# Kernel optimization log

Measured on AMD Instinct MI355X. Metric: run time of the kernel, lower is better.

The kernel has to match this reference:

```python
import jax, jax.numpy as jnp
import numpy as np

B, LX, LM, D = 4, 512, 512, 256

def setup_inputs() -> dict:
    key = jax.random.key(0)
    ks = jax.random.split(key, 7)
    s = 1.0 / np.sqrt(D)
    return {
        "x": jax.random.normal(ks[0], (B, LX, D), jnp.float32),
        "memory": jax.random.normal(ks[1], (B, LM, D), jnp.float32),
        "memory_mask": jax.random.randint(ks[2], (B, LM), 0, 2, jnp.int32),
        "W1": jax.random.normal(ks[3], (D, D), jnp.float32) * s,
        "b1": jax.random.normal(ks[4], (D,), jnp.float32) * s,
        "W2": jax.random.normal(ks[5], (D, D), jnp.float32) * s,
        "Wt": jax.random.normal(ks[6], (D,), jnp.float32) * s,
    }

def reference(x, memory, memory_mask, W1, b1, W2, Wt):
    # item1: (B, Lx, D); item2: (B, Lm, D)
    item1 = jnp.einsum("bxd,ed->bxe", x, W1) + b1
    item2 = jnp.einsum("bmd,ed->bme", memory, W2)
    # additive attention: tanh of broadcast sum, then reduce D to scalar logit
    item = item1[:, :, None, :] + item2[:, None, :, :]  # (B, Lx, Lm, D)
    S_logit = jnp.einsum("bxmd,d->bxm", jnp.tanh(item), Wt)
    S_logit = jnp.where(memory_mask[:, None, :] == 0, jnp.float32(-10000.0), S_logit)
    return S_logit
```

## Files before the change

kernel.cpp:

```cpp
#include <hip/hip_runtime.h>

namespace {

constexpr int B = 4, LX = 512, LM = 512, D = 256;
constexpr float KSCALE = 2.8853900817779268f;
constexpr float CLAMP = 15.0f;

typedef __attribute__((ext_vector_type(8))) short short8;
typedef __attribute__((ext_vector_type(4))) float f32x4;

__device__ __forceinline__ short f2bf_rne(float f) {
    unsigned u = __float_as_uint(f);
    u += 0x7FFFu + ((u >> 16) & 1u);
    return (short)(u >> 16);
}

__global__ __launch_bounds__(256) void proj_mfma(
    const float* __restrict__ x, const float* __restrict__ mem,
    const float* __restrict__ W1, const float* __restrict__ b1,
    const float* __restrict__ W2, float* __restrict__ E1, float* __restrict__ E2)
{
    const int tid  = threadIdx.x;
    const int wv   = tid >> 6;
    const int lane = tid & 63;
    const int tile = blockIdx.x * 4 + wv;
    const int z    = tile >> 11;
    const int t    = tile & 2047;
    const int r0   = (t >> 4) << 4;
    const int e0   = (t & 15) << 4;
    const int lr   = lane & 15;
    const int quad = lane >> 4;

    const float* __restrict__ A = (z ? mem : x) + (size_t)(r0 + lr) * D + quad * 8;
    const float* __restrict__ W = (z ? W2 : W1) + (size_t)(e0 + lr) * D + quad * 8;

    f32x4 acc = {0.f, 0.f, 0.f, 0.f};
#pragma unroll
    for (int kc = 0; kc < D; kc += 32) {
        float4 a0 = *(const float4*)(A + kc);
        float4 a1 = *(const float4*)(A + kc + 4);
        float4 w0 = *(const float4*)(W + kc);
        float4 w1 = *(const float4*)(W + kc + 4);
        short8 af, bf;
        af[0] = f2bf_rne(a0.x); af[1] = f2bf_rne(a0.y);
        af[2] = f2bf_rne(a0.z); af[3] = f2bf_rne(a0.w);
        af[4] = f2bf_rne(a1.x); af[5] = f2bf_rne(a1.y);
        af[6] = f2bf_rne(a1.z); af[7] = f2bf_rne(a1.w);
        bf[0] = f2bf_rne(w0.x); bf[1] = f2bf_rne(w0.y);
        bf[2] = f2bf_rne(w0.z); bf[3] = f2bf_rne(w0.w);
        bf[4] = f2bf_rne(w1.x); bf[5] = f2bf_rne(w1.y);
        bf[6] = f2bf_rne(w1.z); bf[7] = f2bf_rne(w1.w);
        acc = __builtin_amdgcn_mfma_f32_16x16x32_bf16(af, bf, acc, 0, 0, 0);
    }

    float* __restrict__ E = z ? E2 : E1;
    const float bias = z ? 0.f : b1[e0 + lr];
#pragma unroll
    for (int reg = 0; reg < 4; ++reg) {
        const int row = quad * 4 + reg;
        float arg = KSCALE * (acc[reg] + bias);
        arg = fminf(fmaxf(arg, -CLAMP), CLAMP);
        E[(size_t)(r0 + row) * D + e0 + lr] = __builtin_amdgcn_exp2f(arg);
    }
}

__global__ __launch_bounds__(256) void tanh_score_kernel(
    const float* __restrict__ e1p, const float* __restrict__ e2p,
    const float* __restrict__ Wt, const int* __restrict__ mask,
    float* __restrict__ out)
{
    const int tid = threadIdx.x;
    const int b = blockIdx.z;
    const int x0 = blockIdx.y * 32;
    const int m0 = blockIdx.x * 32;

    __shared__ float sA[32][132];
    __shared__ float sB[32][132];

    const int tx = tid & 15, ty = tid >> 4;
    const int srow = tid >> 3;
    const int sc = (tid & 7) * 16;

    float acc00 = 0.f, acc01 = 0.f, acc10 = 0.f, acc11 = 0.f, accW = 0.f;

    for (int c = 0; c < 2; ++c) {
        const int dB = c * 128;
        const float* gA = &e1p[((size_t)b * LX + x0 + srow) * D + dB + sc];
        const float* gB = &e2p[((size_t)b * LM + m0 + srow) * D + dB + sc];
        float4 A0 = *(const float4*)(gA + 0);
        float4 A1 = *(const float4*)(gA + 4);
        float4 A2 = *(const float4*)(gA + 8);
        float4 A3 = *(const float4*)(gA + 12);
        float4 B0 = *(const float4*)(gB + 0);
        float4 B1 = *(const float4*)(gB + 4);
        float4 B2 = *(const float4*)(gB + 8);
        float4 B3 = *(const float4*)(gB + 12);
        __syncthreads();
        *(float4*)&sA[srow][sc + 0]  = A0;
        *(float4*)&sA[srow][sc + 4]  = A1;
        *(float4*)&sA[srow][sc + 8]  = A2;
        *(float4*)&sA[srow][sc + 12] = A3;
        *(float4*)&sB[srow][sc + 0]  = B0;
        *(float4*)&sB[srow][sc + 4]  = B1;
        *(float4*)&sB[srow][sc + 8]  = B2;
        *(float4*)&sB[srow][sc + 12] = B3;
        __syncthreads();

#pragma unroll 4
        for (int d = 0; d < 128; d += 4) {
            const float4 wq  = *(const float4*)&Wt[dB + d];
            const float4 ra0 = *(const float4*)&sA[ty][d];
            const float4 ra1 = *(const float4*)&sA[ty + 16][d];
            const float4 rb0 = *(const float4*)&sB[tx][d];
            const float4 rb1 = *(const float4*)&sB[tx + 16][d];
            accW += (wq.x + wq.y) + (wq.z + wq.w);

#define QUAD(ra, rb, accv) {                                           \
            const float A0 = fmaf((ra).x, (rb).x, 1.f);                \
            const float A1 = fmaf((ra).y, (rb).y, 1.f);                \
            const float A2 = fmaf((ra).z, (rb).z, 1.f);                \
            const float A3 = fmaf((ra).w, (rb).w, 1.f);                \
            const float L = A0 * A1, R = A2 * A3;                      \
            const float den = L * R;                                   \
            const float t0 = fmaf(wq.y, A0, wq.x * A1);                \
            const float t1 = fmaf(wq.w, A2, wq.z * A3);                \
            const float N = fmaf(t1, L, t0 * R);                       \
            (accv) = fmaf(N, __builtin_amdgcn_rcpf(den), (accv)); }

            QUAD(ra0, rb0, acc00);
            QUAD(ra0, rb1, acc01);
            QUAD(ra1, rb0, acc10);
            QUAD(ra1, rb1, acc11);
#undef QUAD
        }
    }

    const int mA = m0 + tx, mB = m0 + tx + 16;
    const int xA = x0 + ty, xB = x0 + ty + 16;
    const bool k0 = mask[b * LM + mA] != 0;
    const bool k1 = mask[b * LM + mB] != 0;
    const float s00 = accW - 2.f * acc00;
    const float s01 = accW - 2.f * acc01;
    const float s10 = accW - 2.f * acc10;
    const float s11 = accW - 2.f * acc11;
    out[((size_t)b * LX + xA) * LM + mA] = k0 ? s00 : -10000.f;
    out[((size_t)b * LX + xA) * LM + mB] = k1 ? s01 : -10000.f;
    out[((size_t)b * LX + xB) * LM + mA] = k0 ? s10 : -10000.f;
    out[((size_t)b * LX + xB) * LM + mB] = k1 ? s11 : -10000.f;
}

}

extern "C" void kernel_launch(void* const* d_in, const int* in_sizes, int n_in,
                              void* d_out, int out_size, void* d_ws, size_t ws_size,
                              hipStream_t stream)
{
    const float* x    = (const float*)d_in[0];
    const float* mem  = (const float*)d_in[1];
    const int*   mask = (const int*)d_in[2];
    const float* W1   = (const float*)d_in[3];
    const float* b1   = (const float*)d_in[4];
    const float* W2   = (const float*)d_in[5];
    const float* Wt   = (const float*)d_in[6];
    float* out = (float*)d_out;

    float* E1 = (float*)d_ws;
    float* E2 = E1 + (size_t)B * LX * D;

    proj_mfma<<<dim3(1024), 256, 0, stream>>>(x, mem, W1, b1, W2, E1, E2);

    tanh_score_kernel<<<dim3(LM / 32, LX / 32, B), 256, 0, stream>>>(
        E1, E2, Wt, mask, out);
}
```

Before: 112.7 us.

## Stage projection tiles in LDS and enlarge score tile to 32x64

The projection kernel now loads 32-row by 64-column blocks into shared memory as packed bf16, and each wave issues two MFMAs per k-step, reusing its A fragment. This replaces per-wave direct global loads that re-read the weights. The score kernel widens its tile from 32x32 to 32x64 and stages D in 64-wide chunks, so each thread computes 8 outputs. This amortizes shared-memory loads of the A rows and the Wt reads, at the cost of more registers and half as many blocks.

```diff
diff --git a/kernel.cpp b/kernel.cpp
--- a/kernel.cpp
+++ b/kernel.cpp
@@ -9,58 +9,70 @@
 typedef __attribute__((ext_vector_type(8))) short short8;
 typedef __attribute__((ext_vector_type(4))) float f32x4;
 
-__device__ __forceinline__ short f2bf_rne(float f) {
+__device__ __forceinline__ unsigned bfbits(float f) {
     unsigned u = __float_as_uint(f);
     u += 0x7FFFu + ((u >> 16) & 1u);
-    return (short)(u >> 16);
+    return u >> 16;
+}
+__device__ __forceinline__ int pack2(float a, float b) {
+    return (int)(bfbits(a) | (bfbits(b) << 16));
 }
 
 __global__ __launch_bounds__(256) void proj_mfma(
     const float* __restrict__ x, const float* __restrict__ mem,
-    const float* __restrict__ W1, const float* __restrict__ b1,
+    const float* __restrict__ W1, const float* __restrict__ b1v,
     const float* __restrict__ W2, float* __restrict__ E1, float* __restrict__ E2)
 {
-    const int tid  = threadIdx.x;
-    const int wv   = tid >> 6;
-    const int lane = tid & 63;
-    const int tile = blockIdx.x * 4 + wv;
-    const int z    = tile >> 11;
-    const int t    = tile & 2047;
-    const int r0   = (t >> 4) << 4;
-    const int e0   = (t & 15) << 4;
-    const int lr   = lane & 15;
-    const int quad = lane >> 4;
+    const int tid = threadIdx.x;
+    const int m0c = blockIdx.x * 32;
+    const int e0  = blockIdx.y * 64;
+    const int z   = m0c >= 2048;
+    const int r0  = z ? (m0c - 2048) : m0c;
+    const float* __restrict__ A = (z ? mem : x) + (size_t)r0 * D;
+    const float* __restrict__ W = z ? W2 : W1;
+    float* __restrict__ E = z ? E2 : E1;
 
-    const float* __restrict__ A = (z ? mem : x) + (size_t)(r0 + lr) * D + quad * 8;
-    const float* __restrict__ W = (z ? W2 : W1) + (size_t)(e0 + lr) * D + quad * 8;
+    __shared__ short sA[32][40];
+    __shared__ short sW[64][40];
 
-    f32x4 acc = {0.f, 0.f, 0.f, 0.f};
-#pragma unroll
+    const int wv = tid >> 6, lane = tid & 63;
+    const int lr = lane & 15, quad = lane >> 4;
+    const int g   = wv & 1;
+    const int cg0 = (wv >> 1) * 2;
+
+    const int srA = tid >> 3;
+    const int scA = (tid & 7) * 4;
+
+    f32x4 acc0 = {0.f, 0.f, 0.f, 0.f};
+    f32x4 acc1 = {0.f, 0.f, 0.f, 0.f};
+
     for (int kc = 0; kc < D; kc += 32) {
-        float4 a0 = *(const float4*)(A + kc);
-        float4 a1 = *(const float4*)(A + kc + 4);
-        float4 w0 = *(const float4*)(W + kc);
-        float4 w1 = *(const float4*)(W + kc + 4);
-        short8 af, bf;
-        af[0] = f2bf_rne(a0.x); af[1] = f2bf_rne(a0.y);
-        af[2] = f2bf_rne(a0.z); af[3] = f2bf_rne(a0.w);
-        af[4] = f2bf_rne(a1.x); af[5] = f2bf_rne(a1.y);
-        af[6] = f2bf_rne(a1.z); af[7] = f2bf_rne(a1.w);
-        bf[0] = f2bf_rne(w0.x); bf[1] = f2bf_rne(w0.y);
-        bf[2] = f2bf_rne(w0.z); bf[3] = f2bf_rne(w0.w);
-        bf[4] = f2bf_rne(w1.x); bf[5] = f2bf_rne(w1.y);
-        bf[6] = f2bf_rne(w1.z); bf[7] = f2bf_rne(w1.w);
-        acc = __builtin_amdgcn_mfma_f32_16x16x32_bf16(af, bf, acc, 0, 0, 0);
+        float4 av = *(const float4*)&A[(size_t)srA * D + kc + scA];
+        float4 w0 = *(const float4*)&W[(size_t)(e0 + srA) * D + kc + scA];
+        float4 w1 = *(const float4*)&W[(size_t)(e0 + 32 + srA) * D + kc + scA];
+        __syncthreads();
+        *(int2*)&sA[srA][scA]      = make_int2(pack2(av.x, av.y), pack2(av.z, av.w));
+        *(int2*)&sW[srA][scA]      = make_int2(pack2(w0.x, w0.y), pack2(w0.z, w0.w));
+        *(int2*)&sW[srA + 32][scA] = make_int2(pack2(w1.x, w1.y), pack2(w1.z, w1.w));
+        __syncthreads();
+        short8 af  = *(const short8*)&sA[g * 16 + lr][quad * 8];
+        short8 bf0 = *(const short8*)&sW[cg0 * 16 + lr][quad * 8];
+        short8 bf1 = *(const short8*)&sW[cg0 * 16 + 16 + lr][quad * 8];
+        acc0 = __builtin_amdgcn_mfma_f32_16x16x32_bf16(af, bf0, acc0, 0, 0, 0);
+        acc1 = __builtin_amdgcn_mfma_f32_16x16x32_bf16(af, bf1, acc1, 0, 0, 0);
     }
 
-    float* __restrict__ E = z ? E2 : E1;
-    const float bias = z ? 0.f : b1[e0 + lr];
+    const float bias0 = z ? 0.f : b1v[e0 + cg0 * 16 + lr];
+    const float bias1 = z ? 0.f : b1v[e0 + cg0 * 16 + 16 + lr];
 #pragma unroll
     for (int reg = 0; reg < 4; ++reg) {
-        const int row = quad * 4 + reg;
-        float arg = KSCALE * (acc[reg] + bias);
-        arg = fminf(fmaxf(arg, -CLAMP), CLAMP);
-        E[(size_t)(r0 + row) * D + e0 + lr] = __builtin_amdgcn_exp2f(arg);
+        const int row = r0 + g * 16 + quad * 4 + reg;
+        float a0 = KSCALE * (acc0[reg] + bias0);
+        float a1 = KSCALE * (acc1[reg] + bias1);
+        a0 = fminf(fmaxf(a0, -CLAMP), CLAMP);
+        a1 = fminf(fmaxf(a1, -CLAMP), CLAMP);
+        E[(size_t)row * D + e0 + cg0 * 16 + lr]      = __builtin_amdgcn_exp2f(a0);
+        E[(size_t)row * D + e0 + cg0 * 16 + 16 + lr] = __builtin_amdgcn_exp2f(a1);
     }
 }
 
@@ -70,83 +82,83 @@
     float* __restrict__ out)
 {
     const int tid = threadIdx.x;
-    const int b = blockIdx.z;
+    const int b  = blockIdx.z;
     const int x0 = blockIdx.y * 32;
-    const int m0 = blockIdx.x * 32;
+    const int m0 = blockIdx.x * 64;
 
-    __shared__ float sA[32][132];
-    __shared__ float sB[32][132];
+    __shared__ float sA[32][68];
+    __shared__ float sB[64][68];
 
     const int tx = tid & 15, ty = tid >> 4;
-    const int srow = tid >> 3;
-    const int sc = (tid & 7) * 16;
+    const int rA = tid >> 3, cA = (tid & 7) * 8;
+    const int rB = tid >> 2, cB = (tid & 3) * 16;
 
-    float acc00 = 0.f, acc01 = 0.f, acc10 = 0.f, acc11 = 0.f, accW = 0.f;
+    float a00 = 0.f, a01 = 0.f, a02 = 0.f, a03 = 0.f;
+    float a10 = 0.f, a11 = 0.f, a12 = 0.f, a13 = 0.f;
+    float accW = 0.f;
 
-    for (int c = 0; c < 2; ++c) {
-        const int dB = c * 128;
-        const float* gA = &e1p[((size_t)b * LX + x0 + srow) * D + dB + sc];
-        const float* gB = &e2p[((size_t)b * LM + m0 + srow) * D + dB + sc];
+    for (int c = 0; c < 4; ++c) {
+        const int dB = c * 64;
+        const float* gA = &e1p[((size_t)b * LX + x0 + rA) * D + dB + cA];
+        const float* gB = &e2p[((size_t)b * LM + m0 + rB) * D + dB + cB];
         float4 A0 = *(const float4*)(gA + 0);
         float4 A1 = *(const float4*)(gA + 4);
-        float4 A2 = *(const float4*)(gA + 8);
-        float4 A3 = *(const float4*)(gA + 12);
         float4 B0 = *(const float4*)(gB + 0);
         float4 B1 = *(const float4*)(gB + 4);
         float4 B2 = *(const float4*)(gB + 8);
         float4 B3 = *(const float4*)(gB + 12);
         __syncthreads();
-        *(float4*)&sA[srow][sc + 0]  = A0;
-        *(float4*)&sA[srow][sc + 4]  = A1;
-        *(float4*)&sA[srow][sc + 8]  = A2;
-        *(float4*)&sA[srow][sc + 12] = A3;
-        *(float4*)&sB[srow][sc + 0]  = B0;
-        *(float4*)&sB[srow][sc + 4]  = B1;
-        *(float4*)&sB[srow][sc + 8]  = B2;
-        *(float4*)&sB[srow][sc + 12] = B3;
+        *(float4*)&sA[rA][cA + 0] = A0;
+        *(float4*)&sA[rA][cA + 4] = A1;
+        *(float4*)&sB[rB][cB + 0]  = B0;
+        *(float4*)&sB[rB][cB + 4]  = B1;
+        *(float4*)&sB[rB][cB + 8]  = B2;
+        *(float4*)&sB[rB][cB + 12] = B3;
         __syncthreads();
 
 #pragma unroll 4
-        for (int d = 0; d < 128; d += 4) {
+        for (int d = 0; d < 64; d += 4) {
             const float4 wq  = *(const float4*)&Wt[dB + d];
             const float4 ra0 = *(const float4*)&sA[ty][d];
             const float4 ra1 = *(const float4*)&sA[ty + 16][d];
             const float4 rb0 = *(const float4*)&sB[tx][d];
             const float4 rb1 = *(const float4*)&sB[tx + 16][d];
+            const float4 rb2 = *(const float4*)&sB[tx + 32][d];
+            const float4 rb3 = *(const float4*)&sB[tx + 48][d];
             accW += (wq.x + wq.y) + (wq.z + wq.w);
 
 #define QUAD(ra, rb, accv) {                                           \
-            const float A0 = fmaf((ra).x, (rb).x, 1.f);                \
-            const float A1 = fmaf((ra).y, (rb).y, 1.f);                \
-            const float A2 = fmaf((ra).z, (rb).z, 1.f);                \
-            const float A3 = fmaf((ra).w, (rb).w, 1.f);                \
-            const float L = A0 * A1, R = A2 * A3;                      \
-            const float den = L * R;                                   \
-            const float t0 = fmaf(wq.y, A0, wq.x * A1);                \
-            const float t1 = fmaf(wq.w, A2, wq.z * A3);                \
-            const float N = fmaf(t1, L, t0 * R);                       \
-            (accv) = fmaf(N, __builtin_amdgcn_rcpf(den), (accv)); }
+            const float A0_ = fmaf((ra).x, (rb).x, 1.f);               \
+            const float A1_ = fmaf((ra).y, (rb).y, 1.f);               \
+            const float A2_ = fmaf((ra).z, (rb).z, 1.f);               \
+            const float A3_ = fmaf((ra).w, (rb).w, 1.f);               \
+            const float L_ = A0_ * A1_, R_ = A2_ * A3_;                \
+            const float den_ = L_ * R_;                                \
+            const float t0_ = fmaf(wq.y, A0_, wq.x * A1_);             \
+            const float t1_ = fmaf(wq.w, A2_, wq.z * A3_);             \
+            const float N_ = fmaf(t1_, L_, t0_ * R_);                  \
+            (accv) = fmaf(N_, __builtin_amdgcn_rcpf(den_), (accv)); }
 
-            QUAD(ra0, rb0, acc00);
-            QUAD(ra0, rb1, acc01);
-            QUAD(ra1, rb0, acc10);
-            QUAD(ra1, rb1, acc11);
+            QUAD(ra0, rb0, a00); QUAD(ra0, rb1, a01);
+            QUAD(ra0, rb2, a02); QUAD(ra0, rb3, a03);
+            QUAD(ra1, rb0, a10); QUAD(ra1, rb1, a11);
+            QUAD(ra1, rb2, a12); QUAD(ra1, rb3, a13);
 #undef QUAD
         }
     }
 
-    const int mA = m0 + tx, mB = m0 + tx + 16;
     const int xA = x0 + ty, xB = x0 + ty + 16;
-    const bool k0 = mask[b * LM + mA] != 0;
-    const bool k1 = mask[b * LM + mB] != 0;
-    const float s00 = accW - 2.f * acc00;
-    const float s01 = accW - 2.f * acc01;
-    const float s10 = accW - 2.f * acc10;
-    const float s11 = accW - 2.f * acc11;
-    out[((size_t)b * LX + xA) * LM + mA] = k0 ? s00 : -10000.f;
-    out[((size_t)b * LX + xA) * LM + mB] = k1 ? s01 : -10000.f;
-    out[((size_t)b * LX + xB) * LM + mA] = k0 ? s10 : -10000.f;
-    out[((size_t)b * LX + xB) * LM + mB] = k1 ? s11 : -10000.f;
+    const int mm[4] = {m0 + tx, m0 + tx + 16, m0 + tx + 32, m0 + tx + 48};
+    float s0[4] = {accW - 2.f * a00, accW - 2.f * a01,
+                   accW - 2.f * a02, accW - 2.f * a03};
+    float s1[4] = {accW - 2.f * a10, accW - 2.f * a11,
+                   accW - 2.f * a12, accW - 2.f * a13};
+#pragma unroll
+    for (int k = 0; k < 4; ++k) {
+        const bool keep = mask[b * LM + mm[k]] != 0;
+        out[((size_t)b * LX + xA) * LM + mm[k]] = keep ? s0[k] : -10000.f;
+        out[((size_t)b * LX + xB) * LM + mm[k]] = keep ? s1[k] : -10000.f;
+    }
 }
 
 }
@@ -167,8 +179,8 @@
     float* E1 = (float*)d_ws;
     float* E2 = E1 + (size_t)B * LX * D;
 
-    proj_mfma<<<dim3(1024), 256, 0, stream>>>(x, mem, W1, b1, W2, E1, E2);
+    proj_mfma<<<dim3(128, 4), 256, 0, stream>>>(x, mem, W1, b1, W2, E1, E2);
 
-    tanh_score_kernel<<<dim3(LM / 32, LX / 32, B), 256, 0, stream>>>(
+    tanh_score_kernel<<<dim3(LM / 64, LX / 32, B), 256, 0, stream>>>(
         E1, E2, Wt, mask, out);
 }
```

New measurement: 104.8 us. 1.08x faster.
